# Kernel optimization log

Measured on AMD Instinct MI355X. Metric: run time of the kernel, lower is better.

The kernel has to match this reference:

```python
import jax, jax.numpy as jnp
import numpy as np
from jax import lax

IN_CH = 32
OUT_CH = 32
K = 7
PAD = 3
STRIDE = 1


def setup_inputs() -> dict:
    key = jax.random.key(0)
    k1, k2, k3 = jax.random.split(key, 3)
    B, T = 4, 4096
    x = jax.random.normal(k1, (B, IN_CH, T), dtype=jnp.float32)
    # weight-generating conv params: [out*in*k, in, k]
    fan_in = IN_CH * K
    W = jax.random.normal(k2, (OUT_CH * IN_CH * K, IN_CH, K), dtype=jnp.float32) / np.sqrt(fan_in).astype(np.float32)
    b = jax.random.normal(k3, (OUT_CH * IN_CH * K,), dtype=jnp.float32) * 0.01
    return {"x": x, "W": W, "b": b}


def _unfold1d(x):
    # x: [B, C, L]; pad then stack K shifted views -> [B, C, K, T]
    xp = jnp.pad(x, ((0, 0), (0, 0), (PAD, PAD)))
    Lp = xp.shape[-1]
    T = Lp - K + 1
    return jnp.stack([xp[:, :, i:i + T:STRIDE] for i in range(K)], axis=2)


def reference(x, W, b):
    B, C, L = x.shape
    # dynamic weight generation: conv1d, same padding -> [B, out*in*K, T]
    dw = lax.conv_general_dilated(
        x, W, window_strides=(STRIDE,), padding=[(PAD, PAD)],
        dimension_numbers=("NCH", "OIH", "NCH"))
    dw = dw + b[None, :, None]
    dw = dw.reshape(B, OUT_CH, IN_CH, K, -1)  # [B, O, I, K, T]
    dw = jax.nn.softmax(dw / np.sqrt(K).astype(np.float32), axis=3)
    x_unf = _unfold1d(x)  # [B, I, K, T]
    y = jnp.einsum("bckt,bockt->bot", x_unf, dw)
    return y
```

## Files before the change

kernel.cpp:

```cpp
#include <hip/hip_runtime.h>
#include <hip/hip_bf16.h>


typedef unsigned short u16;
typedef unsigned int u32;
typedef __attribute__((ext_vector_type(8))) short short8;
typedef __attribute__((ext_vector_type(4))) float f32x4;

#define IN_CH 32
#define OUT_CH 32
#define KW 7
#define TSZ 4096
#define BSZ 4
#define CONTR 224
#define NROWS 7168
#define BLK_T 512
#define XS_STRIDE 40
#define XS_ROWS (BLK_T + 6)
#define SLICE_U16 3584
#define CH_U16 25088
#define CEXP2 0.54528747f

__device__ __forceinline__ u32 f2bf(float v) {
    u32 b = __float_as_uint(v);
    return (b + 0x7fffu + ((b >> 16) & 1u)) >> 16;
}

__device__ __forceinline__ void glds16(const u16* g, u16* l) {
    __builtin_amdgcn_global_load_lds((__attribute__((address_space(1))) void*)g,
                                     (__attribute__((address_space(3))) void*)l,
                                     16, 0, 0);
}

__global__ __launch_bounds__(256)
void wprep(const float* __restrict__ W, const float* __restrict__ bias,
           u16* __restrict__ Wp, float* __restrict__ bp) {
    int idx = blockIdx.x * 256 + threadIdx.x;
    if (idx < NROWS * CONTR) {
        int e  = idx & 7;
        int pp = (idx >> 3) & 3;
        int t1 = idx >> 5;
        int rp = t1 % 112;
        int t2 = t1 / 112;
        int j  = t2 % 7;
        int ch = t2 / 7;
        int p  = pp ^ ((rp >> 1) & 3);
        int c  = p * 8 + e;
        int k  = rp >> 4;
        int q  = rp & 15;
        int gp = ch * 16 + q;
        int o  = gp >> 5;
        int i  = gp & 31;
        int grow = (o * IN_CH + i) * KW + k;
        Wp[idx] = (u16)f2bf(W[(size_t)grow * CONTR + c * KW + j]);
    }
    if (idx < NROWS) {
        int rp = idx % 112;
        int ch = idx / 112;
        int k = rp >> 4, q = rp & 15;
        int gp = ch * 16 + q;
        int o = gp >> 5, i = gp & 31;
        bp[idx] = bias[(o * IN_CH + i) * KW + k];
    }
}

__global__ __launch_bounds__(256)
void xprep(const float* __restrict__ x, u16* __restrict__ xT) {
    int bid = blockIdx.x;
    int b = bid >> 6;
    int t0 = (bid & 63) * 64;
    __shared__ float lds[32][65];
    int tid = threadIdx.x;
    #pragma unroll
    for (int it = 0; it < 8; ++it) {
        int gi = it * 256 + tid;
        int c = gi >> 6;
        int t = gi & 63;
        lds[c][t] = x[((size_t)b * IN_CH + c) * TSZ + t0 + t];
    }
    __syncthreads();
    #pragma unroll
    for (int it = 0; it < 4; ++it) {
        int wi = it * 256 + tid;
        int t  = wi >> 4;
        int cp = wi & 15;
        u32 b0 = f2bf(lds[cp * 2][t]);
        u32 b1 = f2bf(lds[cp * 2 + 1][t]);
        ((u32*)xT)[((size_t)b * TSZ + t0 + t) * 16 + cp] = b0 | (b1 << 16);
    }
}

__global__ __launch_bounds__(512, 1)
void dconv_main(const u16* __restrict__ Wp, const float* __restrict__ bp,
                const u16* __restrict__ xT, float* __restrict__ out) {
    __shared__ u16 xs[XS_ROWS * XS_STRIDE];
    __shared__ u16 wbuf[2][CH_U16];

    int tid  = threadIdx.x;
    int lane = tid & 63;
    int wave = tid >> 6;
    int g    = lane >> 4;
    int col  = lane & 15;

    int bid = blockIdx.x;
    int b   = bid & 3;
    int tt  = (bid >> 2) & 7;
    int os  = bid >> 5;
    int t0  = tt * BLK_T;

    #pragma unroll
    for (int it = 0; it < 17; ++it) {
        int wi = it * 512 + tid;
        if (wi < XS_ROWS * 16) {
            int row = wi >> 4;
            int cp  = wi & 15;
            int t = t0 - 3 + row;
            u32 v = 0;
            if (t >= 0 && t < TSZ)
                v = ((const u32*)xT)[((size_t)b * TSZ + t) * 16 + cp];
            *(u32*)&xs[row * XS_STRIDE + cp * 2] = v;
        }
    }

    if (wave < 7) {
        const u16* src = Wp + (size_t)(os * 8) * CH_U16 + wave * SLICE_U16 + lane * 8;
        u16* dst = &wbuf[0][wave * SLICE_U16];
        #pragma unroll
        for (int it = 0; it < 7; ++it) glds16(src + it * 512, dst + it * 512);
    }
    __syncthreads();

    int laneA = col * 32 + ((g ^ ((col >> 1) & 3)) * 8);
    int colw0 = wave * 64 + col;

    float yacc[4] = {0.f, 0.f, 0.f, 0.f};

    #pragma unroll 1
    for (int ci = 0; ci < 8; ++ci) {
        int cur = ci & 1;
        if (ci < 7 && wave < 7) {
            const u16* src = Wp + (size_t)(os * 8 + ci + 1) * CH_U16 + wave * SLICE_U16 + lane * 8;
            u16* dst = &wbuf[cur ^ 1][wave * SLICE_U16];
            #pragma unroll
            for (int it = 0; it < 7; ++it) glds16(src + it * 512, dst + it * 512);
        }

        int ch = os * 8 + ci;
        int cc = ci & 1;

        f32x4 acc[7][4];
        const float* bsrc = bp + ch * 112 + g * 4;
        #pragma unroll
        for (int m = 0; m < 7; ++m) {
            f32x4 bv = *(const f32x4*)(bsrc + m * 16);
            acc[m][0] = bv; acc[m][1] = bv; acc[m][2] = bv; acc[m][3] = bv;
        }

        const u16* wl = &wbuf[cur][laneA];
        #pragma unroll
        for (int j = 0; j < 7; ++j) {
            short8 bf[4];
            #pragma unroll
            for (int ct = 0; ct < 4; ++ct)
                bf[ct] = *(const short8*)&xs[(colw0 + ct * 16 + j) * XS_STRIDE + g * 8];
            #pragma unroll
            for (int m = 0; m < 7; ++m) {
                short8 af = *(const short8*)(wl + j * SLICE_U16 + m * 512);
                acc[m][0] = __builtin_amdgcn_mfma_f32_16x16x32_bf16(af, bf[0], acc[m][0], 0, 0, 0);
                acc[m][1] = __builtin_amdgcn_mfma_f32_16x16x32_bf16(af, bf[1], acc[m][1], 0, 0, 0);
                acc[m][2] = __builtin_amdgcn_mfma_f32_16x16x32_bf16(af, bf[2], acc[m][2], 0, 0, 0);
                acc[m][3] = __builtin_amdgcn_mfma_f32_16x16x32_bf16(af, bf[3], acc[m][3], 0, 0, 0);
            }
        }

        int ibase = cc * 16 + g * 4;
        #pragma unroll
        for (int ct = 0; ct < 4; ++ct) {
            int colw = colw0 + ct * 16;
            u32 xv0[7], xv1[7];
            #pragma unroll
            for (int k = 0; k < 7; ++k) {
                const u32* px = (const u32*)&xs[(colw + k) * XS_STRIDE + ibase];
                xv0[k] = px[0]; xv1[k] = px[1];
            }
            #pragma unroll
            for (int r = 0; r < 4; ++r) {
                float ssum = 0.f, psum = 0.f;
                #pragma unroll
                for (int k = 0; k < 7; ++k) {
                    float e = __builtin_amdgcn_exp2f(acc[k][ct][r] * CEXP2);
                    u32 w = (r & 2) ? xv1[k] : xv0[k];
                    float xf = __uint_as_float((r & 1) ? (w & 0xffff0000u) : (w << 16));
                    ssum += e;
                    psum = fmaf(e, xf, psum);
                }
                yacc[ct] += psum * __builtin_amdgcn_rcpf(ssum);
            }
        }

        if (cc == 1) {
            int o = os * 4 + (ci >> 1);
            #pragma unroll
            for (int ct = 0; ct < 4; ++ct) {
                float v = yacc[ct];
                v += __shfl_xor(v, 16, 64);
                v += __shfl_xor(v, 32, 64);
                if (lane < 16)
                    out[((size_t)b * OUT_CH + o) * TSZ + t0 + wave * 64 + ct * 16 + col] = v;
                yacc[ct] = 0.f;
            }
        }
        __syncthreads();
    }
}

extern "C" void kernel_launch(void* const* d_in, const int* in_sizes, int n_in,
                              void* d_out, int out_size, void* d_ws, size_t ws_size,
                              hipStream_t stream) {
    const float* x    = (const float*)d_in[0];
    const float* W    = (const float*)d_in[1];
    const float* bias = (const float*)d_in[2];
    float* out = (float*)d_out;

    u16*   Wp = (u16*)d_ws;
    float* bp = (float*)((char*)d_ws + 3211264);
    u16*   xT = (u16*)((char*)d_ws + 3211264 + 28672);

    hipLaunchKernelGGL(wprep, dim3(6272), dim3(256), 0, stream, W, bias, Wp, bp);
    hipLaunchKernelGGL(xprep, dim3(BSZ * (TSZ / 64)), dim3(256), 0, stream, x, xT);
    hipLaunchKernelGGL(dconv_main, dim3(256), dim3(512), 0, stream, Wp, bp, xT, out);
}
```

Baseline: 122.3 us.

## Stage weight chunks in LDS for coalesced repacking and move loop barrier earlier

Result: no change. 124.4 us (+1.7%).

```diff
diff --git a/kernel.cpp b/kernel.cpp
--- a/kernel.cpp
+++ b/kernel.cpp
@@ -32,35 +32,37 @@
                                      16, 0, 0);
 }
 
-__global__ __launch_bounds__(256)
+__global__ __launch_bounds__(512)
 void wprep(const float* __restrict__ W, const float* __restrict__ bias,
            u16* __restrict__ Wp, float* __restrict__ bp) {
-    int idx = blockIdx.x * 256 + threadIdx.x;
-    if (idx < NROWS * CONTR) {
-        int e  = idx & 7;
-        int pp = (idx >> 3) & 3;
-        int t1 = idx >> 5;
+    __shared__ float ws[CH_U16];
+    int ch  = blockIdx.x;
+    int tid = threadIdx.x;
+    const float* src = W + (size_t)ch * CH_U16;
+    #pragma unroll
+    for (int it = 0; it < 49; ++it)
+        ws[it * 512 + tid] = src[it * 512 + tid];
+    __syncthreads();
+    u16* dst = Wp + (size_t)ch * CH_U16;
+    #pragma unroll
+    for (int it = 0; it < 49; ++it) {
+        int oidx = it * 512 + tid;
+        int e  = oidx & 7;
+        int pp = (oidx >> 3) & 3;
+        int t1 = oidx >> 5;
         int rp = t1 % 112;
-        int t2 = t1 / 112;
-        int j  = t2 % 7;
-        int ch = t2 / 7;
+        int j  = t1 / 112;
         int p  = pp ^ ((rp >> 1) & 3);
         int c  = p * 8 + e;
         int k  = rp >> 4;
         int q  = rp & 15;
-        int gp = ch * 16 + q;
-        int o  = gp >> 5;
-        int i  = gp & 31;
-        int grow = (o * IN_CH + i) * KW + k;
-        Wp[idx] = (u16)f2bf(W[(size_t)grow * CONTR + c * KW + j]);
-    }
-    if (idx < NROWS) {
-        int rp = idx % 112;
-        int ch = idx / 112;
-        int k = rp >> 4, q = rp & 15;
+        dst[oidx] = (u16)f2bf(ws[(q * 7 + k) * CONTR + c * 7 + j]);
+    }
+    if (tid < 112) {
+        int k = tid >> 4, q = tid & 15;
         int gp = ch * 16 + q;
         int o = gp >> 5, i = gp & 31;
-        bp[idx] = bias[(o * IN_CH + i) * KW + k];
+        bp[ch * 112 + tid] = bias[(o * IN_CH + i) * KW + k];
     }
 }
 
@@ -172,6 +174,8 @@
                 acc[m][3] = __builtin_amdgcn_mfma_f32_16x16x32_bf16(af, bf[3], acc[m][3], 0, 0, 0);
             }
         }
+
+        __syncthreads();
 
         int ibase = cc * 16 + g * 4;
         #pragma unroll
@@ -210,7 +214,6 @@
                 yacc[ct] = 0.f;
             }
         }
-        __syncthreads();
     }
 }
 
@@ -226,7 +229,7 @@
     float* bp = (float*)((char*)d_ws + 3211264);
     u16*   xT = (u16*)((char*)d_ws + 3211264 + 28672);
 
-    hipLaunchKernelGGL(wprep, dim3(6272), dim3(256), 0, stream, W, bias, Wp, bp);
+    hipLaunchKernelGGL(wprep, dim3(64), dim3(512), 0, stream, W, bias, Wp, bp);
     hipLaunchKernelGGL(xprep, dim3(BSZ * (TSZ / 64)), dim3(256), 0, stream, x, xT);
     hipLaunchKernelGGL(dconv_main, dim3(256), dim3(512), 0, stream, Wp, bp, xT, out);
 }
```
